# Kernel optimization log

Measured on AMD Instinct MI355X. Metric: run time of the kernel, lower is better.

The kernel has to match this reference:

```python
import jax, jax.numpy as jnp
import numpy as np

V, E, H, B, S, O, L = 50257, 256, 512, 64, 1024, 1, 2


def setup_inputs() -> dict:
    key = jax.random.key(0)
    ks = jax.random.split(key, 16)
    s = 0.02
    d = {
        "tokens": jax.random.randint(ks[0], (B, S), 0, V),
        "emb": jax.random.normal(ks[1], (V, E), jnp.float32) * s,
        "fc_w": jax.random.normal(ks[2], (O, H), jnp.float32) * s,
        "fc_b": jnp.zeros((O,), jnp.float32),
    }
    ins = [E, H]
    for l in range(L):
        i = ins[l]
        d[f"gate_w{l}"] = jax.random.normal(ks[3 + 4 * l], (2 * H, i + H), jnp.float32) * s
        d[f"gate_b{l}"] = jnp.zeros((2 * H,), jnp.float32)
        d[f"gi_w{l}"] = jax.random.normal(ks[4 + 4 * l], (H, i), jnp.float32) * s
        d[f"gi_b{l}"] = jnp.zeros((H,), jnp.float32)
        d[f"gh_w{l}"] = jax.random.normal(ks[5 + 4 * l], (H, H), jnp.float32) * s
        d[f"gh_b{l}"] = jnp.zeros((H,), jnp.float32)
    return d


def _cell(x, h, gw, gb, giw, gib, ghw, ghb):
    # gates from concat(input, hidden): [B, 2H]
    gates = jnp.concatenate([x, h], axis=-1) @ gw.T + gb
    r, z = jnp.split(gates, 2, axis=-1)
    r = jax.nn.sigmoid(r)
    z = jax.nn.sigmoid(z)
    n = jnp.tanh(x @ giw.T + gib + r * (h @ ghw.T + ghb))
    return (1.0 - z) * n + z * h  # dropout is identity at inference


def _forward(tokens, emb, fc_w, fc_b, layers):
    x = emb[tokens]  # [B, S, E]
    b = tokens.shape[0]
    h0 = tuple(jnp.zeros((b, H), x.dtype) for _ in layers)

    def step(hs, xt):  # xt: [B, E]
        new = []
        inp = xt
        for h, p in zip(hs, layers):
            h = _cell(inp, h, *p)
            new.append(h)
            inp = h
        return tuple(new), None

    hs, _ = jax.lax.scan(step, h0, jnp.swapaxes(x, 0, 1))  # scan over S
    out = hs[-1] @ fc_w.T + fc_b  # [B, 1]
    return jax.nn.sigmoid(jnp.squeeze(out))  # [B]


def reference(tokens, emb, fc_w, fc_b,
              gate_w0, gate_b0, gi_w0, gi_b0, gh_w0, gh_b0,
              gate_w1, gate_b1, gi_w1, gi_b1, gh_w1, gh_b1):
    layers = [
        (gate_w0, gate_b0, gi_w0, gi_b0, gh_w0, gh_b0),
        (gate_w1, gate_b1, gi_w1, gi_b1, gh_w1, gh_b1),
    ]
    return _forward(tokens, emb, fc_w, fc_b, layers)
```

## Files before the change

kernel.cpp:

```cpp
#include <hip/hip_runtime.h>

typedef _Float16 f16;
typedef _Float16 f16x8 __attribute__((ext_vector_type(8)));
typedef float f32x4 __attribute__((ext_vector_type(4)));
typedef unsigned long long u64;

#define B_ 64
#define S_ 1024
#define E_ 256
#define H_ 512
#define NG 1536
#define TCH 128
#define NCHUNK (S_/TCH)
#define ROWS_CH (TCH*B_)
#define HS_LD 544

__device__ __forceinline__ float sigm(float x) { return 1.f / (1.f + __expf(-x)); }

#define ALOAD(p) __hip_atomic_load((p), __ATOMIC_RELAXED, __HIP_MEMORY_SCOPE_AGENT)
#define ASTORE(p, v) __hip_atomic_store((p), (v), __ATOMIC_RELAXED, __HIP_MEMORY_SCOPE_AGENT)

__global__ __launch_bounds__(256) void k_embed(const int* __restrict__ tok,
        const float* __restrict__ emb, f16* __restrict__ X, int t0) {
    int idx = blockIdx.x * 256 + threadIdx.x;
    int r = idx >> 6;
    int c4 = (idx & 63) << 2;
    int t = t0 + (r >> 6), b = r & 63;
    int tk = tok[b * S_ + t];
    float4 v = *reinterpret_cast<const float4*>(emb + (size_t)tk * E_ + c4);
    union { f16 h[4]; u64 u; } w;
    w.h[0] = (f16)v.x; w.h[1] = (f16)v.y; w.h[2] = (f16)v.z; w.h[3] = (f16)v.w;
    *reinterpret_cast<u64*>(X + (size_t)r * E_ + c4) = w.u;
}

__global__ __launch_bounds__(256) void k_packW(const float* __restrict__ gw, int ld, int off,
        const float* __restrict__ g2, f16* __restrict__ W, int KK) {
    int idx = blockIdx.x * 256 + threadIdx.x;
    int per = KK >> 2;
    if (idx >= NG * per) return;
    int row = idx / per;
    int c4 = (idx % per) << 2;
    const float* src = (row < 1024) ? gw + (size_t)row * ld + off + c4
                                    : g2 + (size_t)(row - 1024) * KK + c4;
    float4 v = *reinterpret_cast<const float4*>(src);
    union { f16 h[4]; u64 u; } w;
    w.h[0] = (f16)v.x; w.h[1] = (f16)v.y; w.h[2] = (f16)v.z; w.h[3] = (f16)v.w;
    *reinterpret_cast<u64*>(W + (size_t)row * KK + c4) = w.u;
}

__global__ __launch_bounds__(256) void k_packBias(const float* __restrict__ gb,
        const float* __restrict__ gib, float* __restrict__ bias) {
    int i = blockIdx.x * 256 + threadIdx.x;
    if (i < 1024) bias[i] = gb[i];
    else if (i < NG) bias[i] = gib[i - 1024];
}

__global__ __launch_bounds__(256) void k_gemm(const f16* __restrict__ A,
        const f16* __restrict__ Bm, const float* __restrict__ bias,
        f16* __restrict__ C, int K) {
    __shared__ f16 As[64][40];
    __shared__ f16 Bs[64][40];
    const int tid = threadIdx.x;
    const int m0 = blockIdx.y << 6, n0 = blockIdx.x << 6;
    const int w = tid >> 6, l = tid & 63;
    const int wr = (w >> 1) << 5, wc = (w & 1) << 5;
    const int srow = tid >> 2, sc8 = (tid & 3) << 3;
    const int fr = l & 15, kl = (l >> 4) << 3;
    f32x4 acc[2][2] = {};
    for (int k0 = 0; k0 < K; k0 += 32) {
        *reinterpret_cast<f16x8*>(&As[srow][sc8]) =
            *reinterpret_cast<const f16x8*>(A + (size_t)(m0 + srow) * K + k0 + sc8);
        *reinterpret_cast<f16x8*>(&Bs[srow][sc8]) =
            *reinterpret_cast<const f16x8*>(Bm + (size_t)(n0 + srow) * K + k0 + sc8);
        __syncthreads();
        f16x8 a0 = *reinterpret_cast<const f16x8*>(&As[wr + fr][kl]);
        f16x8 a1 = *reinterpret_cast<const f16x8*>(&As[wr + 16 + fr][kl]);
        f16x8 b0 = *reinterpret_cast<const f16x8*>(&Bs[wc + fr][kl]);
        f16x8 b1 = *reinterpret_cast<const f16x8*>(&Bs[wc + 16 + fr][kl]);
        acc[0][0] = __builtin_amdgcn_mfma_f32_16x16x32_f16(a0, b0, acc[0][0], 0, 0, 0);
        acc[0][1] = __builtin_amdgcn_mfma_f32_16x16x32_f16(a0, b1, acc[0][1], 0, 0, 0);
        acc[1][0] = __builtin_amdgcn_mfma_f32_16x16x32_f16(a1, b0, acc[1][0], 0, 0, 0);
        acc[1][1] = __builtin_amdgcn_mfma_f32_16x16x32_f16(a1, b1, acc[1][1], 0, 0, 0);
        __syncthreads();
    }
    for (int fm = 0; fm < 2; ++fm)
        for (int fn = 0; fn < 2; ++fn) {
            int col = n0 + wc + (fn << 4) + fr;
            float bv = bias[col];
            for (int j = 0; j < 4; ++j) {
                int rowg = m0 + wr + (fm << 4) + ((l >> 4) << 2) + j;
                C[(size_t)rowg * NG + col] = (f16)(acc[fm][fn][j] + bv);
            }
        }
}

__global__ __launch_bounds__(256, 1) void k_recur4(
        const f16* __restrict__ Wh0p, const f16* __restrict__ Wh1p,
        const f16* __restrict__ Z0, const f16* __restrict__ Z1,
        const float* __restrict__ ghb0, const float* __restrict__ ghb1,
        u64* ring0, u64* ring1, f16* __restrict__ H0out, f16* __restrict__ h1out,
        int t00, int n0, int t01, int n1) {
    __shared__ __align__(16) f16 HS[8][HS_LD];
    __shared__ __align__(16) f16 hx[8][40];
    const int blk = blockIdx.x;
    const int c = blk & 7;
    const int l = (blk >> 3) & 1;
    const int gg = blk >> 4;
    const int nsteps = l ? n1 : n0;
    if (nsteps <= 0) return;
    const int t0 = l ? t01 : t00;
    const f16* __restrict__ Wh = l ? Wh1p : Wh0p;
    const f16* __restrict__ Z  = l ? Z1 : Z0;
    const float* __restrict__ ghb = l ? ghb1 : ghb0;
    u64* ring = l ? ring1 : ring0;

    const int i0 = gg << 5;
    const int tid = threadIdx.x;
    const int w = tid >> 6;
    const int lane = tid & 63;
    const int colb = lane & 15;
    const int bq = lane & 7;
    const int j4 = lane >> 4;
    const int rrow = lane & 15;
    const int ol = rrow >> 2, gate = rrow & 3;

    f16x8 wA[2][16];
    #pragma unroll
    for (int tl = 0; tl < 2; ++tl) {
        const int out = i0 + (w << 3) + (tl << 2) + ol;
        #pragma unroll
        for (int t = 0; t < 16; ++t) {
            f16x8 v{};
            if (gate < 3)
                v = *reinterpret_cast<const f16x8*>(
                        Wh + ((size_t)(gate * H_ + out)) * H_ + (t << 5) + (j4 << 3));
            wA[tl][t] = v;
        }
    }
    const int outA = i0 + (w << 3) + j4;
    const int outB = outA + 4;
    const float gbA = ghb[outA], gbB = ghb[outB];

    for (int sl = 0; sl < nsteps; ++sl) {
        const int s = t0 + sl;
        const size_t zrow = ((size_t)sl * 64 + (c << 3) + bq) * NG;
        float zrA = (float)Z[zrow + outA];
        float zzA = (float)Z[zrow + H_ + outA];
        float znA = (float)Z[zrow + 2 * H_ + outA];
        float zrB = (float)Z[zrow + outB];
        float zzB = (float)Z[zrow + H_ + outB];
        float znB = (float)Z[zrow + 2 * H_ + outB];
        {
            const u64* src = ring + ((size_t)(s & 3) * 8 + c) * 2048;
            u64 g[8];
            #pragma unroll
            for (int i = 0; i < 8; ++i) g[i] = ALOAD(src + (i << 8) + tid);
            unsigned miss = 0;
            #pragma unroll
            for (int i = 0; i < 8; ++i) {
                if ((unsigned)(g[i] >> 32) == (unsigned)s) {
                    *reinterpret_cast<unsigned*>(
                        &HS[i][((tid >> 4) << 5) + ((tid & 15) << 1)]) = (unsigned)g[i];
                } else miss |= 1u << i;
            }
            while (miss) {
                #pragma unroll
                for (int i = 0; i < 8; ++i)
                    if (miss & (1u << i)) g[i] = ALOAD(src + (i << 8) + tid);
                #pragma unroll
                for (int i = 0; i < 8; ++i)
                    if ((miss & (1u << i)) && (unsigned)(g[i] >> 32) == (unsigned)s) {
                        *reinterpret_cast<unsigned*>(
                            &HS[i][((tid >> 4) << 5) + ((tid & 15) << 1)]) = (unsigned)g[i];
                        miss &= ~(1u << i);
                    }
            }
        }
        __syncthreads();
        f32x4 a00{}, a01{}, a10{}, a11{};
        #pragma unroll
        for (int t = 0; t < 16; ++t) {
            f16x8 bf = *reinterpret_cast<const f16x8*>(&HS[bq][(t << 5) + (j4 << 3)]);
            if (t & 1) {
                a01 = __builtin_amdgcn_mfma_f32_16x16x32_f16(wA[0][t], bf, a01, 0, 0, 0);
                a11 = __builtin_amdgcn_mfma_f32_16x16x32_f16(wA[1][t], bf, a11, 0, 0, 0);
            } else {
                a00 = __builtin_amdgcn_mfma_f32_16x16x32_f16(wA[0][t], bf, a00, 0, 0, 0);
                a10 = __builtin_amdgcn_mfma_f32_16x16x32_f16(wA[1][t], bf, a10, 0, 0, 0);
            }
        }
        f32x4 dA = a00 + a01;
        f32x4 dB = a10 + a11;
        if (colb < 8) {
            float holdA = (float)HS[bq][outA];
            float holdB = (float)HS[bq][outB];
            float rA = sigm(zrA + dA[0]);
            float zA = sigm(zzA + dA[1]);
            float nA = tanhf(znA + rA * (dA[2] + gbA));
            float rB = sigm(zrB + dB[0]);
            float zB = sigm(zzB + dB[1]);
            float nB = tanhf(znB + rB * (dB[2] + gbB));
            hx[bq][(w << 3) + j4]     = (f16)((1.f - zA) * nA + zA * holdA);
            hx[bq][(w << 3) + 4 + j4] = (f16)((1.f - zB) * nB + zB * holdB);
        }
        __syncthreads();
        if (tid < 128) {
            const int b = tid >> 4, d = tid & 15;
            unsigned dval = *reinterpret_cast<const unsigned*>(&hx[b][d << 1]);
            u64 gr = ((u64)(unsigned)(s + 1) << 32) | (u64)dval;
            ASTORE(ring + ((size_t)((s + 1) & 3) * 8 + c) * 2048
                        + ((size_t)b << 8) + (gg << 4) + d, gr);
            if (l == 0)
                *reinterpret_cast<unsigned*>(
                    &H0out[((size_t)sl * 64 + (c << 3) + b) * H_ + i0 + (d << 1)]) = dval;
            else if (s == S_ - 1)
                *reinterpret_cast<unsigned*>(
                    &h1out[((size_t)(c << 3) + b) * H_ + i0 + (d << 1)]) = dval;
        }
        __syncthreads();
    }
}

__global__ __launch_bounds__(64) void k_final(const f16* __restrict__ h,
        const float* __restrict__ fcw, const float* __restrict__ fcb,
        float* __restrict__ out) {
    int b = threadIdx.x;
    float acc = fcb[0];
    for (int k = 0; k < H_; ++k) acc += (float)h[(size_t)b * H_ + k] * fcw[k];
    out[b] = sigm(acc);
}

extern "C" void kernel_launch(void* const* d_in, const int* in_sizes, int n_in,
                              void* d_out, int out_size, void* d_ws, size_t ws_size,
                              hipStream_t stream) {
    (void)in_sizes; (void)n_in; (void)out_size; (void)ws_size;
    const int*   tokens = (const int*)d_in[0];
    const float* emb  = (const float*)d_in[1];
    const float* fc_w = (const float*)d_in[2];
    const float* fc_b = (const float*)d_in[3];
    const float* gw0  = (const float*)d_in[4];
    const float* gb0  = (const float*)d_in[5];
    const float* giw0 = (const float*)d_in[6];
    const float* gib0 = (const float*)d_in[7];
    const float* ghw0 = (const float*)d_in[8];
    const float* ghb0 = (const float*)d_in[9];
    const float* gw1  = (const float*)d_in[10];
    const float* gb1  = (const float*)d_in[11];
    const float* giw1 = (const float*)d_in[12];
    const float* gib1 = (const float*)d_in[13];
    const float* ghw1 = (const float*)d_in[14];
    const float* ghb1 = (const float*)d_in[15];

    char* base = (char*)d_ws;
    size_t off = 0;
    auto carve = [&](size_t bytes) {
        char* p = base + off;
        off = (off + bytes + 255) & ~(size_t)255;
        return p;
    };
    f16*   Wx0   = (f16*)carve((size_t)NG * 256 * 2);
    f16*   Wh0   = (f16*)carve((size_t)NG * 512 * 2);
    f16*   Wx1   = (f16*)carve((size_t)NG * 512 * 2);
    f16*   Wh1   = (f16*)carve((size_t)NG * 512 * 2);
    float* bias0 = (float*)carve(NG * 4);
    float* bias1 = (float*)carve(NG * 4);
    u64*   ring0 = (u64*)carve((size_t)4 * 8 * 2048 * 8);
    u64*   ring1 = (u64*)carve((size_t)4 * 8 * 2048 * 8);
    f16*   h1out = (f16*)carve((size_t)B_ * H_ * 2);
    f16*   Xc    = (f16*)carve((size_t)ROWS_CH * 256 * 2);
    f16*   Zc0   = (f16*)carve((size_t)ROWS_CH * NG * 2);
    f16*   H0c   = (f16*)carve((size_t)ROWS_CH * 512 * 2);
    f16*   Zc1   = (f16*)carve((size_t)ROWS_CH * NG * 2);

    hipMemsetAsync(ring0, 0, (size_t)4 * 8 * 2048 * 8, stream);
    hipMemsetAsync(ring1, 0, (size_t)4 * 8 * 2048 * 8, stream);

    k_packW<<<384, 256, 0, stream>>>(gw0, 768, 0,    giw0, Wx0, 256);
    k_packW<<<768, 256, 0, stream>>>(gw0, 768, 256,  ghw0, Wh0, 512);
    k_packW<<<768, 256, 0, stream>>>(gw1, 1024, 0,   giw1, Wx1, 512);
    k_packW<<<768, 256, 0, stream>>>(gw1, 1024, 512, ghw1, Wh1, 512);
    k_packBias<<<6, 256, 0, stream>>>(gb0, gib0, bias0);
    k_packBias<<<6, 256, 0, stream>>>(gb1, gib1, bias1);

    dim3 gemmGrid(NG / 64, ROWS_CH / 64);
    for (int ch = 0; ch < NCHUNK; ++ch) {
        int t0 = ch * TCH;
        k_embed<<<ROWS_CH * 64 / 256, 256, 0, stream>>>(tokens, emb, Xc, t0);
        k_gemm<<<gemmGrid, 256, 0, stream>>>(Xc, Wx0, bias0, Zc0, 256);
        k_recur4<<<256, 256, 0, stream>>>(Wh0, Wh1, Zc0, Zc1, ghb0, ghb1,
                                          ring0, ring1, H0c, h1out,
                                          t0, TCH, t0 - TCH, ch ? TCH : 0);
        k_gemm<<<gemmGrid, 256, 0, stream>>>(H0c, Wx1, bias1, Zc1, 512);
    }
    k_recur4<<<256, 256, 0, stream>>>(Wh0, Wh1, Zc0, Zc1, ghb0, ghb1,
                                      ring0, ring1, H0c, h1out,
                                      0, 0, (NCHUNK - 1) * TCH, TCH);
    k_final<<<1, 64, 0, stream>>>(h1out, fc_w, fc_b, (float*)d_out);
}
```

Before: 2.778 ms.

## Fuse embedding gather into layer-0 input GEMM and double-buffer recurrence staging

```diff
diff --git a/kernel.cpp b/kernel.cpp
--- a/kernel.cpp
+++ b/kernel.cpp
@@ -10,6 +10,7 @@
 #define E_ 256
 #define H_ 512
 #define NG 1536
+#define V_ 50257
 #define TCH 128
 #define NCHUNK (S_/TCH)
 #define ROWS_CH (TCH*B_)
@@ -20,17 +21,14 @@
 #define ALOAD(p) __hip_atomic_load((p), __ATOMIC_RELAXED, __HIP_MEMORY_SCOPE_AGENT)
 #define ASTORE(p, v) __hip_atomic_store((p), (v), __ATOMIC_RELAXED, __HIP_MEMORY_SCOPE_AGENT)
 
-__global__ __launch_bounds__(256) void k_embed(const int* __restrict__ tok,
-        const float* __restrict__ emb, f16* __restrict__ X, int t0) {
-    int idx = blockIdx.x * 256 + threadIdx.x;
-    int r = idx >> 6;
-    int c4 = (idx & 63) << 2;
-    int t = t0 + (r >> 6), b = r & 63;
-    int tk = tok[b * S_ + t];
-    float4 v = *reinterpret_cast<const float4*>(emb + (size_t)tk * E_ + c4);
+__global__ __launch_bounds__(256) void k_embconv(const float* __restrict__ emb,
+        f16* __restrict__ out) {
+    long long i = (long long)blockIdx.x * 256 + threadIdx.x;
+    if (i >= (long long)V_ * E_ / 4) return;
+    float4 v = reinterpret_cast<const float4*>(emb)[i];
     union { f16 h[4]; u64 u; } w;
     w.h[0] = (f16)v.x; w.h[1] = (f16)v.y; w.h[2] = (f16)v.z; w.h[3] = (f16)v.w;
-    *reinterpret_cast<u64*>(X + (size_t)r * E_ + c4) = w.u;
+    reinterpret_cast<u64*>(out)[i] = w.u;
 }
 
 __global__ __launch_bounds__(256) void k_packW(const float* __restrict__ gw, int ld, int off,
@@ -94,6 +92,48 @@
         }
 }
 
+__global__ __launch_bounds__(256) void k_gemmE(const int* __restrict__ tok, int t0,
+        const f16* __restrict__ embh, const f16* __restrict__ Bm,
+        const float* __restrict__ bias, f16* __restrict__ C) {
+    __shared__ f16 As[64][40];
+    __shared__ f16 Bs[64][40];
+    const int tid = threadIdx.x;
+    const int m0 = blockIdx.y << 6, n0 = blockIdx.x << 6;
+    const int w = tid >> 6, l = tid & 63;
+    const int wr = (w >> 1) << 5, wc = (w & 1) << 5;
+    const int srow = tid >> 2, sc8 = (tid & 3) << 3;
+    const int fr = l & 15, kl = (l >> 4) << 3;
+    const int grow = m0 + srow;
+    const int tk = tok[(grow & 63) * S_ + t0 + (grow >> 6)];
+    const f16* arow = embh + (size_t)tk * E_;
+    f32x4 acc[2][2] = {};
+    for (int k0 = 0; k0 < E_; k0 += 32) {
+        *reinterpret_cast<f16x8*>(&As[srow][sc8]) =
+            *reinterpret_cast<const f16x8*>(arow + k0 + sc8);
+        *reinterpret_cast<f16x8*>(&Bs[srow][sc8]) =
+            *reinterpret_cast<const f16x8*>(Bm + (size_t)(n0 + srow) * E_ + k0 + sc8);
+        __syncthreads();
+        f16x8 a0 = *reinterpret_cast<const f16x8*>(&As[wr + fr][kl]);
+        f16x8 a1 = *reinterpret_cast<const f16x8*>(&As[wr + 16 + fr][kl]);
+        f16x8 b0 = *reinterpret_cast<const f16x8*>(&Bs[wc + fr][kl]);
+        f16x8 b1 = *reinterpret_cast<const f16x8*>(&Bs[wc + 16 + fr][kl]);
+        acc[0][0] = __builtin_amdgcn_mfma_f32_16x16x32_f16(a0, b0, acc[0][0], 0, 0, 0);
+        acc[0][1] = __builtin_amdgcn_mfma_f32_16x16x32_f16(a0, b1, acc[0][1], 0, 0, 0);
+        acc[1][0] = __builtin_amdgcn_mfma_f32_16x16x32_f16(a1, b0, acc[1][0], 0, 0, 0);
+        acc[1][1] = __builtin_amdgcn_mfma_f32_16x16x32_f16(a1, b1, acc[1][1], 0, 0, 0);
+        __syncthreads();
+    }
+    for (int fm = 0; fm < 2; ++fm)
+        for (int fn = 0; fn < 2; ++fn) {
+            int col = n0 + wc + (fn << 4) + fr;
+            float bv = bias[col];
+            for (int j = 0; j < 4; ++j) {
+                int rowg = m0 + wr + (fm << 4) + ((l >> 4) << 2) + j;
+                C[(size_t)rowg * NG + col] = (f16)(acc[fm][fn][j] + bv);
+            }
+        }
+}
+
 __global__ __launch_bounds__(256, 1) void k_recur4(
         const f16* __restrict__ Wh0p, const f16* __restrict__ Wh1p,
         const f16* __restrict__ Z0, const f16* __restrict__ Z1,
@@ -101,7 +141,7 @@
         u64* ring0, u64* ring1, f16* __restrict__ H0out, f16* __restrict__ h1out,
         int t00, int n0, int t01, int n1) {
     __shared__ __align__(16) f16 HS[8][HS_LD];
-    __shared__ __align__(16) f16 hx[8][40];
+    __shared__ __align__(16) f16 hx[2][8][40];
     const int blk = blockIdx.x;
     const int c = blk & 7;
     const int l = (blk >> 3) & 1;
@@ -143,6 +183,7 @@
 
     for (int sl = 0; sl < nsteps; ++sl) {
         const int s = t0 + sl;
+        const int p = sl & 1;
         const size_t zrow = ((size_t)sl * 64 + (c << 3) + bq) * NG;
         float zrA = (float)Z[zrow + outA];
         float zzA = (float)Z[zrow + H_ + outA];
@@ -200,13 +241,13 @@
             float rB = sigm(zrB + dB[0]);
             float zB = sigm(zzB + dB[1]);
             float nB = tanhf(znB + rB * (dB[2] + gbB));
-            hx[bq][(w << 3) + j4]     = (f16)((1.f - zA) * nA + zA * holdA);
-            hx[bq][(w << 3) + 4 + j4] = (f16)((1.f - zB) * nB + zB * holdB);
+            hx[p][bq][(w << 3) + j4]     = (f16)((1.f - zA) * nA + zA * holdA);
+            hx[p][bq][(w << 3) + 4 + j4] = (f16)((1.f - zB) * nB + zB * holdB);
         }
         __syncthreads();
         if (tid < 128) {
             const int b = tid >> 4, d = tid & 15;
-            unsigned dval = *reinterpret_cast<const unsigned*>(&hx[b][d << 1]);
+            unsigned dval = *reinterpret_cast<const unsigned*>(&hx[p][b][d << 1]);
             u64 gr = ((u64)(unsigned)(s + 1) << 32) | (u64)dval;
             ASTORE(ring + ((size_t)((s + 1) & 3) * 8 + c) * 2048
                         + ((size_t)b << 8) + (gg << 4) + d, gr);
@@ -217,7 +258,6 @@
                 *reinterpret_cast<unsigned*>(
                     &h1out[((size_t)(c << 3) + b) * H_ + i0 + (d << 1)]) = dval;
         }
-        __syncthreads();
     }
 }
 
@@ -258,6 +298,7 @@
         off = (off + bytes + 255) & ~(size_t)255;
         return p;
     };
+    f16*   embh  = (f16*)carve((size_t)V_ * E_ * 2);
     f16*   Wx0   = (f16*)carve((size_t)NG * 256 * 2);
     f16*   Wh0   = (f16*)carve((size_t)NG * 512 * 2);
     f16*   Wx1   = (f16*)carve((size_t)NG * 512 * 2);
@@ -267,7 +308,6 @@
     u64*   ring0 = (u64*)carve((size_t)4 * 8 * 2048 * 8);
     u64*   ring1 = (u64*)carve((size_t)4 * 8 * 2048 * 8);
     f16*   h1out = (f16*)carve((size_t)B_ * H_ * 2);
-    f16*   Xc    = (f16*)carve((size_t)ROWS_CH * 256 * 2);
     f16*   Zc0   = (f16*)carve((size_t)ROWS_CH * NG * 2);
     f16*   H0c   = (f16*)carve((size_t)ROWS_CH * 512 * 2);
     f16*   Zc1   = (f16*)carve((size_t)ROWS_CH * NG * 2);
@@ -275,6 +315,7 @@
     hipMemsetAsync(ring0, 0, (size_t)4 * 8 * 2048 * 8, stream);
     hipMemsetAsync(ring1, 0, (size_t)4 * 8 * 2048 * 8, stream);
 
+    k_embconv<<<(V_ * E_ / 4 + 255) / 256, 256, 0, stream>>>(emb, embh);
     k_packW<<<384, 256, 0, stream>>>(gw0, 768, 0,    giw0, Wx0, 256);
     k_packW<<<768, 256, 0, stream>>>(gw0, 768, 256,  ghw0, Wh0, 512);
     k_packW<<<768, 256, 0, stream>>>(gw1, 1024, 0,   giw1, Wx1, 512);
@@ -285,8 +326,7 @@
     dim3 gemmGrid(NG / 64, ROWS_CH / 64);
     for (int ch = 0; ch < NCHUNK; ++ch) {
         int t0 = ch * TCH;
-        k_embed<<<ROWS_CH * 64 / 256, 256, 0, stream>>>(tokens, emb, Xc, t0);
-        k_gemm<<<gemmGrid, 256, 0, stream>>>(Xc, Wx0, bias0, Zc0, 256);
+        k_gemmE<<<gemmGrid, 256, 0, stream>>>(tokens, t0, embh, Wx0, bias0, Zc0);
         k_recur4<<<256, 256, 0, stream>>>(Wh0, Wh1, Zc0, Zc1, ghb0, ghb1,
                                           ring0, ring1, H0c, h1out,
                                           t0, TCH, t0 - TCH, ch ? TCH : 0);
```

New measurement: 3.205 ms. 1.15x slower.
